# Kernel tuning notes

Hardware: AMD Instinct MI355X
Metric: run time of the kernel (lower is better)

## Reference

```python
import jax, jax.numpy as jnp
import numpy as np

B, I, H, MS, M = 8192, 1024, 1024, 64, 16
TAU = 1.0


def setup_inputs() -> dict:
    key = jax.random.key(0)
    ks = jax.random.split(key, 24)
    s = 0.02
    eps = 1e-6
    return {
        "x": jax.random.normal(ks[0], (B, I), jnp.float32),
        "h": jax.random.normal(ks[1], (B, H), jnp.float32),
        "c": jax.random.normal(ks[2], (B, H), jnp.float32),
        "memory": jax.random.normal(ks[3], (B, M, MS), jnp.float32),
        "u_gs": jax.random.uniform(ks[4], (B, M), jnp.float32, eps, 1.0 - eps),
        "u_a": jax.random.uniform(ks[5], (B, 1), jnp.float32, eps, 1.0 - eps),
        "u_b": jax.random.uniform(ks[6], (B, 1), jnp.float32, eps, 1.0 - eps),
        # pre-concatenated gate weights, matching torch.cat((W_x2*, W_h2*, W_c2*), 0)
        "W_i": jax.random.normal(ks[7], (I + 2 * H, H), jnp.float32) * s,
        "b_i": jnp.zeros((H,), jnp.float32),
        "W_f": jax.random.normal(ks[8], (I + 2 * H, H), jnp.float32) * s,
        "b_f": jnp.ones((H,), jnp.float32),
        "W_o": jax.random.normal(ks[9], (I + 2 * H, H), jnp.float32) * s,
        "b_o": jnp.zeros((H,), jnp.float32),
        "W_cand": jax.random.normal(ks[10], (I + H, H), jnp.float32) * s,
        "b_cand": jnp.zeros((H,), jnp.float32),
        "W_m": jax.random.normal(ks[11], (H, MS), jnp.float32) * s,
        "b_m": jnp.zeros((MS,), jnp.float32),
        "w_a_h": jax.random.normal(ks[12], (H, 1), jnp.float32) * s,
        "w_a_x": jax.random.normal(ks[13], (I, 1), jnp.float32) * s,
        "w_a_r": jax.random.normal(ks[14], (MS, 1), jnp.float32) * s,
        "w_b_h": jax.random.normal(ks[15], (H, 1), jnp.float32) * s,
        "w_b_x": jax.random.normal(ks[16], (I, 1), jnp.float32) * s,
        "w_b_r": jax.random.normal(ks[17], (MS, 1), jnp.float32) * s,
    }


def reference(x, h, c, memory, u_gs, u_a, u_b,
              W_i, b_i, W_f, b_f, W_o, b_o, W_cand, b_cand,
              W_m, b_m, w_a_h, w_a_x, w_a_r, w_b_h, w_b_x, w_b_r):
    # LSTM-style gates with peephole c in the concatenated input
    xhc = jnp.concatenate([x, h, c], axis=1)            # [B, I+2H]
    i = jax.nn.sigmoid(xhc @ W_i + b_i)
    f = jax.nn.sigmoid(xhc @ W_f + b_f)
    cp = jnp.tanh(jnp.concatenate([x, h], axis=1) @ W_cand + b_cand)
    c_new = f * c + i * cp
    o = jax.nn.sigmoid(jnp.concatenate([x, h, c_new], axis=1) @ W_o + b_o)
    h_new = o * jnp.tanh(c_new)

    # memory-slot attention with Gumbel-softmax sampling
    micro = h_new @ W_m + b_m                           # [B, MS]
    logits = jnp.einsum('bmk,bk->bm', memory, micro)    # [B, M]
    g = -jnp.log(-jnp.log(u_gs))                        # Gumbel(0,1)
    attn = jax.nn.softmax((logits + g) / TAU, axis=-1)  # sampled_locations
    sampled = jnp.einsum('bmk,bm->bk', memory, attn) + 1.0  # [B, MS]

    # gumbel-sigmoid (binary concrete) for alpha / beta
    la = jnp.log(u_a) - jnp.log1p(-u_a)
    lb = jnp.log(u_b) - jnp.log1p(-u_b)
    alpha = jax.nn.sigmoid((h_new @ w_a_h + x @ w_a_x + sampled @ w_a_r + la) / TAU)
    beta = jax.nn.sigmoid((h_new @ w_b_h + x @ w_b_x + sampled @ w_b_r + lb) / TAU)

    # [B, 2H+2]
    return jnp.concatenate([h_new, c_new, alpha, beta], axis=1)
```

## Files before the change

kernel.cpp:

```cpp
#include <hip/hip_runtime.h>

typedef __bf16 bfrag __attribute__((ext_vector_type(8)));
typedef float f32x4 __attribute__((ext_vector_type(4)));

#define GLDS16(g, l) __builtin_amdgcn_global_load_lds( \
    (__attribute__((address_space(1))) void*)(g),      \
    (__attribute__((address_space(3))) void*)(l), 16, 0, 0)

__device__ __forceinline__ float bf2f(ushort u) {
    return __uint_as_float(((unsigned)u) << 16);
}
__device__ __forceinline__ ushort f2bf(float f) {
    unsigned u = __float_as_uint(f);
    u += 0x7fff + ((u >> 16) & 1);
    return (ushort)(u >> 16);
}
__device__ __forceinline__ float sigmoidf_(float v) {
    return 1.0f / (1.0f + expf(-v));
}

struct TD { const float* src; ushort* dst; int src_ld; int dst_ld; int ktiles; int off; };
struct TA { TD d[6]; };

__global__ __launch_bounds__(256) void k_prep(const float* __restrict__ x,
                                              const float* __restrict__ h,
                                              const float* __restrict__ c,
                                              ushort* __restrict__ xhcb, TA a,
                                              const float* __restrict__ bi,
                                              const float* __restrict__ bf_,
                                              const float* __restrict__ bc,
                                              const float* __restrict__ bo,
                                              float* __restrict__ Biasf) {
    __shared__ float tile[64][65];
    int bid = blockIdx.x;
    int t = threadIdx.x;
    if (bid < 12288) {
        int idx = bid * 256 + t;
        int row = idx / 384;
        int c8 = (idx - row * 384) * 8;
        const float* s = (c8 < 1024) ? &x[(size_t)row * 1024 + c8]
                       : (c8 < 2048) ? &h[(size_t)row * 1024 + (c8 - 1024)]
                                     : &c[(size_t)row * 1024 + (c8 - 2048)];
        float4 va = *(const float4*)s;
        float4 vb = *(const float4*)(s + 4);
        ushort tmp[8] = {f2bf(va.x), f2bf(va.y), f2bf(va.z), f2bf(va.w),
                         f2bf(vb.x), f2bf(vb.y), f2bf(vb.z), f2bf(vb.w)};
        *(uint4*)&xhcb[(size_t)idx * 8] = *(uint4*)tmp;
    } else if (bid < 15120) {
        int tb = bid - 12288;
        int ri = 0;
#pragma unroll
        for (int i = 1; i < 6; ++i) ri = (tb >= a.d[i].off) ? i : ri;
        const float* src = a.d[ri].src;
        ushort* dst = a.d[ri].dst;
        int src_ld = a.d[ri].src_ld, dst_ld = a.d[ri].dst_ld;
        int local = tb - a.d[ri].off;
        int bx = local % a.d[ri].ktiles;
        int by = local / a.d[ri].ktiles;
        int k0 = bx * 64, n0 = by * 64;
        int c4 = (t & 15) * 4;
        int r = t >> 4;
#pragma unroll
        for (int i = 0; i < 4; ++i) {
            int rr = r + i * 16;
            float4 v = *(const float4*)&src[(size_t)(k0 + rr) * src_ld + n0 + c4];
            tile[rr][c4 + 0] = v.x; tile[rr][c4 + 1] = v.y;
            tile[rr][c4 + 2] = v.z; tile[rr][c4 + 3] = v.w;
        }
        __syncthreads();
        int kk8 = (t & 7) * 8;
        int nn = t >> 3;
#pragma unroll
        for (int i = 0; i < 2; ++i) {
            int n = nn + i * 32;
            ushort tmp[8];
#pragma unroll
            for (int j = 0; j < 8; ++j) tmp[j] = f2bf(tile[kk8 + j][n]);
            *(uint4*)&dst[(size_t)(n0 + n) * dst_ld + k0 + kk8] = *(uint4*)tmp;
        }
    } else {
        int idx = (bid - 15120) * 256 + t;
        int g = idx >> 10, n = idx & 1023;
        const float* s = (g == 0) ? bi : (g == 1) ? bf_ : (g == 2) ? bc : bo;
        Biasf[idx] = s[n];
    }
}

__global__ __launch_bounds__(512) void k_gemm1(const ushort* __restrict__ xhcb,
                                               const ushort* __restrict__ WT,
                                               const float* __restrict__ bias,
                                               ushort* __restrict__ Pre) {
    __shared__ __align__(16) ushort lds[2][32768];
    const int t = threadIdx.x;
    const int m0 = blockIdx.x * 256;
    const int by = blockIdx.y;
    const int n0 = by * 256;
    const int KTOT = (by < 8) ? 3072 : 2048;
    const int NT = KTOT >> 6;
    const int w = t >> 6, l = t & 63;
    const int wr = w >> 2, wc = w & 3;
    const int lane16 = l & 15, quad = l >> 4;
    const int r7 = lane16 & 7;
    const int rowt = t >> 3;
    const int kg = (t & 7) ^ (rowt & 7);
    const int brow_hi = rowt >> 5, brow_lo = rowt & 31;
    f32x4 acc[8][4] = {};

    const ushort* Ag = xhcb + (size_t)(m0 + rowt) * 3072 + kg * 8;
    const ushort* Bg = WT + (size_t)(n0 + brow_lo) * 3072 + kg * 8;

#define STAGE_A(BUF, PI, KT)                                                       \
    do {                                                                           \
        GLDS16(Ag + (size_t)((PI) * 64) * 3072 + (KT) * 64,                        \
               &lds[BUF][((PI) * 64) * 64] + t * 8);                               \
        GLDS16(Ag + (size_t)((PI) * 64 + 128) * 3072 + (KT) * 64,                  \
               &lds[BUF][((PI) * 64 + 128) * 64] + t * 8);                         \
    } while (0)

#define STAGE_B(BUF, PI, KT)                                                       \
    do {                                                                           \
        GLDS16(Bg + (size_t)((PI) * 32 + brow_hi * 64) * 3072 + (KT) * 64,         \
               &lds[BUF][16384 + ((PI) * 128) * 64] + t * 8);                      \
        GLDS16(Bg + (size_t)((PI) * 32 + (2 + brow_hi) * 64) * 3072 + (KT) * 64,   \
               &lds[BUF][16384 + ((PI) * 128 + 64) * 64] + t * 8);                 \
    } while (0)

#define LDAF(dst, QM, H)                                                                  \
    do {                                                                                  \
        _Pragma("unroll") for (int ii = 0; ii < 4; ++ii)                                  \
            dst[ii] = *(const bfrag*)&Acur[(wr * 128 + (QM) * 64 + ii * 16 + lane16) * 64 + \
                                           ((((H) * 4 + quad) ^ r7) * 8)];                \
    } while (0)

#define LDBF(dst, H)                                                                      \
    do {                                                                                  \
        _Pragma("unroll") for (int jj = 0; jj < 4; ++jj)                                  \
            dst[jj] = *(const bfrag*)&Bcur[((jj >> 1) * 128 + wc * 32 + (jj & 1) * 16 + lane16) * 64 + \
                                           ((((H) * 4 + quad) ^ r7) * 8)];                \
    } while (0)

#define MMH(QM, AH, BH)                                                                   \
    do {                                                                                  \
        __builtin_amdgcn_s_setprio(1);                                                    \
        _Pragma("unroll") for (int ii = 0; ii < 4; ++ii) {                                \
            _Pragma("unroll") for (int jj = 0; jj < 4; ++jj)                              \
                acc[(QM) * 4 + ii][jj] = __builtin_amdgcn_mfma_f32_16x16x32_bf16(         \
                    AH[ii], BH[jj], acc[(QM) * 4 + ii][jj], 0, 0, 0);                     \
        }                                                                                 \
        __builtin_amdgcn_s_setprio(0);                                                    \
    } while (0)

    STAGE_A(0, 0, 0); STAGE_B(0, 0, 0);
    STAGE_A(0, 1, 0); STAGE_B(0, 1, 0);
    STAGE_A(1, 0, 1); STAGE_B(1, 0, 1);
    asm volatile("s_waitcnt vmcnt(4)" ::: "memory");
    __builtin_amdgcn_s_barrier();

    for (int kt = 0; kt < NT; ++kt) {
        const int cur = kt & 1;
        const int nxt = cur ^ 1;
        const ushort* Acur = &lds[cur][0];
        const ushort* Bcur = Acur + 16384;
        bfrag a0h0[4], a0h1[4], a1h0[4], a1h1[4], bh0[4], bh1[4];
        LDAF(a0h0, 0, 0); LDBF(bh0, 0);
        LDAF(a0h1, 0, 1); LDBF(bh1, 1);
        if (kt + 1 < NT) STAGE_A(nxt, 1, kt + 1);
        MMH(0, a0h0, bh0);
        __builtin_amdgcn_s_barrier();
        LDAF(a1h0, 1, 0);
        if (kt + 1 < NT) STAGE_B(nxt, 1, kt + 1);
        MMH(0, a0h1, bh1);
        __builtin_amdgcn_s_barrier();
        LDAF(a1h1, 1, 1);
        if (kt + 2 < NT) STAGE_A(cur, 0, kt + 2);
        MMH(1, a1h0, bh0);
        __builtin_amdgcn_s_barrier();
        if (kt + 2 < NT) STAGE_B(cur, 0, kt + 2);
        MMH(1, a1h1, bh1);
        if (kt + 2 < NT) {
            asm volatile("s_waitcnt vmcnt(4)" ::: "memory");
        } else if (kt + 1 < NT) {
            asm volatile("s_waitcnt vmcnt(0)" ::: "memory");
        }
        __builtin_amdgcn_s_barrier();
    }
#undef MMH
#undef LDBF
#undef LDAF
#undef STAGE_B
#undef STAGE_A

#pragma unroll
    for (int i = 0; i < 8; ++i) {
#pragma unroll
        for (int jj = 0; jj < 4; ++jj) {
            int col = n0 + wc * 64 + (jj >> 1) * 32 + (jj & 1) * 16 + lane16;
            float bv = bias[col];
            int rbase = m0 + wr * 128 + i * 16 + quad * 4;
#pragma unroll
            for (int r = 0; r < 4; ++r)
                Pre[(size_t)(rbase + r) * 4096 + col] = f2bf(acc[i][jj][r] + bv);
        }
    }
}

__global__ __launch_bounds__(256) void k_cnew(const ushort* __restrict__ Pre,
                                              const float* __restrict__ cin,
                                              ushort* __restrict__ Cnewb,
                                              float* __restrict__ out) {
    int idx8 = blockIdx.x * 256 + threadIdx.x;
    int b = idx8 >> 7;
    int n8 = (idx8 & 127) * 8;
    uint4 vi = *(const uint4*)(Pre + (size_t)b * 4096 + n8);
    uint4 vf = *(const uint4*)(Pre + (size_t)b * 4096 + 1024 + n8);
    uint4 vc = *(const uint4*)(Pre + (size_t)b * 4096 + 2048 + n8);
    float4 c0 = *(const float4*)(cin + (size_t)b * 1024 + n8);
    float4 c1 = *(const float4*)(cin + (size_t)b * 1024 + n8 + 4);
    const ushort* pi = (const ushort*)&vi;
    const ushort* pf = (const ushort*)&vf;
    const ushort* pc = (const ushort*)&vc;
    float cv[8] = {c0.x, c0.y, c0.z, c0.w, c1.x, c1.y, c1.z, c1.w};
    float cn[8];
    ushort cb[8];
#pragma unroll
    for (int j = 0; j < 8; ++j) {
        float iv = sigmoidf_(bf2f(pi[j]));
        float fv = sigmoidf_(bf2f(pf[j]));
        float cp = tanhf(bf2f(pc[j]));
        cn[j] = fv * cv[j] + iv * cp;
        cb[j] = f2bf(cn[j]);
    }
    *(uint4*)(Cnewb + (size_t)b * 1024 + n8) = *(uint4*)cb;
    float* orow = out + (size_t)b * 2050 + 1024 + n8;
#pragma unroll
    for (int j = 0; j < 4; ++j)
        *(float2*)(orow + j * 2) = make_float2(cn[j * 2], cn[j * 2 + 1]);
}

__global__ __launch_bounds__(256) void k_gemm2(const ushort* __restrict__ Cnewb,
                                               const ushort* __restrict__ WoCT,
                                               const ushort* __restrict__ Pre,
                                               ushort* __restrict__ Hnewb,
                                               float* __restrict__ out) {
    __shared__ __align__(16) ushort As[128 * 64];
    __shared__ __align__(16) ushort Bs[128 * 64];
    int t = threadIdx.x;
    int m0 = blockIdx.x * 128, n0 = blockIdx.y * 128;
    int w = t >> 6, l = t & 63;
    int wm = (w & 1) * 64, wn = (w >> 1) * 64;
    int lane16 = l & 15, quad = l >> 4;
    int rowt = t >> 3;
    int kg = (t & 7) ^ (rowt & 7);
    int r7 = lane16 & 7;
    f32x4 acc[4][4] = {};

    const ushort* Abase = Cnewb + (size_t)(m0 + rowt) * 1024 + kg * 8;
    const ushort* Bbase = WoCT + (size_t)(n0 + rowt) * 1024 + kg * 8;

    for (int k0 = 0; k0 < 1024; k0 += 64) {
#pragma unroll
        for (int q = 0; q < 4; ++q)
            GLDS16(Abase + (size_t)q * 32 * 1024 + k0, As + q * 2048 + t * 8);
#pragma unroll
        for (int q = 0; q < 4; ++q)
            GLDS16(Bbase + (size_t)q * 32 * 1024 + k0, Bs + q * 2048 + t * 8);
        __syncthreads();
#pragma unroll
        for (int hh = 0; hh < 2; ++hh) {
            int slot8 = ((hh * 4 + quad) ^ r7) * 8;
            bfrag af[4], bfr[4];
#pragma unroll
            for (int i = 0; i < 4; ++i) {
                af[i]  = *(const bfrag*)&As[(wm + i * 16 + lane16) * 64 + slot8];
                bfr[i] = *(const bfrag*)&Bs[(wn + i * 16 + lane16) * 64 + slot8];
            }
#pragma unroll
            for (int i = 0; i < 4; ++i)
#pragma unroll
                for (int j = 0; j < 4; ++j)
                    acc[i][j] = __builtin_amdgcn_mfma_f32_16x16x32_bf16(af[i], bfr[j], acc[i][j], 0, 0, 0);
        }
        __syncthreads();
    }
#pragma unroll
    for (int i = 0; i < 4; ++i) {
#pragma unroll
        for (int j = 0; j < 4; ++j) {
            int col = n0 + wn + j * 16 + lane16;
            int rbase = m0 + wm + i * 16 + quad * 4;
#pragma unroll
            for (int r = 0; r < 4; ++r) {
                int row = rbase + r;
                float opre = acc[i][j][r] + bf2f(Pre[(size_t)row * 4096 + 3072 + col]);
                float o = sigmoidf_(opre);
                float cnv = bf2f(Cnewb[(size_t)row * 1024 + col]);
                float hv = o * tanhf(cnv);
                Hnewb[(size_t)row * 1024 + col] = f2bf(hv);
                out[(size_t)row * 2050 + col] = hv;
            }
        }
    }
}

__global__ __launch_bounds__(256) void k_attn(
    const ushort* __restrict__ Hnewb, const float* __restrict__ outr,
    const float* __restrict__ x, const float* __restrict__ memory,
    const float* __restrict__ u_gs, const float* __restrict__ u_a,
    const float* __restrict__ u_b, const ushort* __restrict__ WmT,
    const float* __restrict__ b_m,
    const float* __restrict__ w_a_h, const float* __restrict__ w_a_x,
    const float* __restrict__ w_a_r, const float* __restrict__ w_b_h,
    const float* __restrict__ w_b_x, const float* __restrict__ w_b_r,
    float* __restrict__ out) {
    __shared__ float sMicro[16 * 64];
    __shared__ float sAttn[16 * 16];
    __shared__ float sSamp[16 * 64];

    int b0 = blockIdx.x * 16;
    int t = threadIdx.x;
    int w = t >> 6, l = t & 63;
    int lane16 = l & 15, quad = l >> 4;

    {
        f32x4 acc = {0.f, 0.f, 0.f, 0.f};
        const ushort* Ab = Hnewb + (size_t)(b0 + lane16) * 1024 + quad * 8;
        const ushort* Bb = WmT + (size_t)(w * 16 + lane16) * 1024 + quad * 8;
#pragma unroll 4
        for (int k0 = 0; k0 < 1024; k0 += 32) {
            bfrag av = *(const bfrag*)(Ab + k0);
            bfrag bv = *(const bfrag*)(Bb + k0);
            acc = __builtin_amdgcn_mfma_f32_16x16x32_bf16(av, bv, acc, 0, 0, 0);
        }
        float bm = b_m[w * 16 + lane16];
#pragma unroll
        for (int r = 0; r < 4; ++r)
            sMicro[(quad * 4 + r) * 64 + w * 16 + lane16] = acc[r] + bm;
    }
    __syncthreads();

    {
        int r = t >> 4, m = t & 15;
        const float4* mem4 = (const float4*)(memory + (size_t)(b0 + r) * 1024 + m * 64);
        float lg = 0.f;
#pragma unroll
        for (int k4 = 0; k4 < 16; ++k4) {
            float4 mv = mem4[k4];
            const float* sm = &sMicro[r * 64 + k4 * 4];
            lg += mv.x * sm[0] + mv.y * sm[1] + mv.z * sm[2] + mv.w * sm[3];
        }
        float u = u_gs[(b0 + r) * 16 + m];
        float z = lg - logf(-logf(u));
        float zm = z;
        for (int off = 8; off; off >>= 1) zm = fmaxf(zm, __shfl_xor(zm, off, 16));
        float p = expf(z - zm);
        float ps = p;
        for (int off = 8; off; off >>= 1) ps += __shfl_xor(ps, off, 16);
        sAttn[r * 16 + m] = p / ps;
    }
    __syncthreads();

#pragma unroll
    for (int q = 0; q < 4; ++q) {
        int r = w * 4 + q;
        const float* mem = memory + (size_t)(b0 + r) * 1024 + l;
        float s = 0.f;
#pragma unroll
        for (int m = 0; m < 16; ++m) s += sAttn[r * 16 + m] * mem[m * 64];
        sSamp[r * 64 + l] = s + 1.0f;
    }
    __syncthreads();

    {
        int r = t >> 4, s16 = t & 15;
        size_t hoff = (size_t)(b0 + r) * 2050;
        size_t xoff = (size_t)(b0 + r) * 1024;
        float za = 0.f, zb = 0.f;
        for (int kk = 0; kk < 64; ++kk) {
            int k = s16 + kk * 16;
            float hv = outr[hoff + k];
            float xv = x[xoff + k];
            za += hv * w_a_h[k] + xv * w_a_x[k];
            zb += hv * w_b_h[k] + xv * w_b_x[k];
        }
#pragma unroll
        for (int k = s16 * 4; k < s16 * 4 + 4; ++k) {
            float sv = sSamp[r * 64 + k];
            za += sv * w_a_r[k];
            zb += sv * w_b_r[k];
        }
        for (int off = 8; off; off >>= 1) {
            za += __shfl_xor(za, off, 16);
            zb += __shfl_xor(zb, off, 16);
        }
        if (s16 == 0) {
            float ua = u_a[b0 + r];
            float ub = u_b[b0 + r];
            float la = logf(ua) - log1pf(-ua);
            float lb = logf(ub) - log1pf(-ub);
            out[(size_t)(b0 + r) * 2050 + 2048] = sigmoidf_(za + la);
            out[(size_t)(b0 + r) * 2050 + 2049] = sigmoidf_(zb + lb);
        }
    }
}

extern "C" void kernel_launch(void* const* d_in, const int* in_sizes, int n_in,
                              void* d_out, int out_size, void* d_ws, size_t ws_size,
                              hipStream_t stream) {
    const float* x      = (const float*)d_in[0];
    const float* h      = (const float*)d_in[1];
    const float* c      = (const float*)d_in[2];
    const float* memory = (const float*)d_in[3];
    const float* u_gs   = (const float*)d_in[4];
    const float* u_a    = (const float*)d_in[5];
    const float* u_b    = (const float*)d_in[6];
    const float* W_i    = (const float*)d_in[7];
    const float* b_i    = (const float*)d_in[8];
    const float* W_f    = (const float*)d_in[9];
    const float* b_f    = (const float*)d_in[10];
    const float* W_o    = (const float*)d_in[11];
    const float* b_o    = (const float*)d_in[12];
    const float* W_cand = (const float*)d_in[13];
    const float* b_cand = (const float*)d_in[14];
    const float* W_m    = (const float*)d_in[15];
    const float* b_m    = (const float*)d_in[16];
    const float* w_a_h  = (const float*)d_in[17];
    const float* w_a_x  = (const float*)d_in[18];
    const float* w_a_r  = (const float*)d_in[19];
    const float* w_b_h  = (const float*)d_in[20];
    const float* w_b_x  = (const float*)d_in[21];
    const float* w_b_r  = (const float*)d_in[22];
    float* out = (float*)d_out;

    char* ws = (char*)d_ws;
    ushort* WT    = (ushort*)(ws);
    ushort* WoCT  = (ushort*)(ws + 25165824);
    ushort* Pre   = (ushort*)(ws + 27262976);
    ushort* xhcb  = (ushort*)(ws + 94371840);
    float*  Biasf = (float*)(ws + 144703488);
    ushort* WmT   = (ushort*)(ws + 144719872);
    ushort* Cnewb = xhcb;
    ushort* Hnewb = WT;

    TA ta;
    ta.d[0] = {W_i,                       WT,                        1024, 3072, 48, 0};
    ta.d[1] = {W_f,                       WT + (size_t)1024 * 3072,  1024, 3072, 48, 768};
    ta.d[2] = {W_cand,                    WT + (size_t)2048 * 3072,  1024, 3072, 32, 1536};
    ta.d[3] = {W_o,                       WT + (size_t)3072 * 3072,  1024, 3072, 32, 2048};
    ta.d[4] = {W_o + (size_t)2048 * 1024, WoCT,                      1024, 1024, 16, 2560};
    ta.d[5] = {W_m,                       WmT,                         64, 1024, 16, 2816};

    k_prep<<<15136, 256, 0, stream>>>(x, h, c, xhcb, ta, b_i, b_f, b_cand, b_o, Biasf);

    k_gemm1<<<dim3(32, 16), 512, 0, stream>>>(xhcb, WT, Biasf, Pre);
    k_cnew<<<4096, 256, 0, stream>>>(Pre, c, Cnewb, out);
    k_gemm2<<<dim3(64, 8), 256, 0, stream>>>(Cnewb, WoCT, Pre, Hnewb, out);
    k_attn<<<512, 256, 0, stream>>>(Hnewb, out, x, memory, u_gs, u_a, u_b, WmT, b_m,
                                    w_a_h, w_a_x, w_a_r, w_b_h, w_b_x, w_b_r, out);
}
```

Measured before the change: 476.2 us.

## Prefetch next k-tile's first A/B fragments during last MFMA phase

Moves the LDS reads of the first A and B fragment set for the next k-tile into the final phase of the current iteration, so they overlap with the last MFMA block instead of stalling at loop start. The vmcnt wait is moved earlier and loosened to guarantee the next buffer's data has landed before those reads. This adds live registers for fragments carried across iterations and depends on the revised wait counts being correct for the staging order.

```diff
diff --git a/kernel.cpp b/kernel.cpp
--- a/kernel.cpp
+++ b/kernel.cpp
@@ -105,6 +105,8 @@
     const int kg = (t & 7) ^ (rowt & 7);
     const int brow_hi = rowt >> 5, brow_lo = rowt & 31;
     f32x4 acc[8][4] = {};
+    bfrag a0h0[4], bh0[4];
+    bfrag a0h1[4], bh1[4], a1h0[4], a1h1[4];
 
     const ushort* Ag = xhcb + (size_t)(m0 + rowt) * 3072 + kg * 8;
     const ushort* Bg = WT + (size_t)(n0 + brow_lo) * 3072 + kg * 8;
@@ -125,18 +127,18 @@
                &lds[BUF][16384 + ((PI) * 128 + 64) * 64] + t * 8);                 \
     } while (0)
 
-#define LDAF(dst, QM, H)                                                                  \
+#define LDAF(dst, BASE, QM, H)                                                            \
     do {                                                                                  \
         _Pragma("unroll") for (int ii = 0; ii < 4; ++ii)                                  \
-            dst[ii] = *(const bfrag*)&Acur[(wr * 128 + (QM) * 64 + ii * 16 + lane16) * 64 + \
-                                           ((((H) * 4 + quad) ^ r7) * 8)];                \
+            dst[ii] = *(const bfrag*)&(BASE)[(wr * 128 + (QM) * 64 + ii * 16 + lane16) * 64 + \
+                                             ((((H) * 4 + quad) ^ r7) * 8)];              \
     } while (0)
 
-#define LDBF(dst, H)                                                                      \
+#define LDBF(dst, BASE, H)                                                                \
     do {                                                                                  \
         _Pragma("unroll") for (int jj = 0; jj < 4; ++jj)                                  \
-            dst[jj] = *(const bfrag*)&Bcur[((jj >> 1) * 128 + wc * 32 + (jj & 1) * 16 + lane16) * 64 + \
-                                           ((((H) * 4 + quad) ^ r7) * 8)];                \
+            dst[jj] = *(const bfrag*)&(BASE)[((jj >> 1) * 128 + wc * 32 + (jj & 1) * 16 + lane16) * 64 + \
+                                             ((((H) * 4 + quad) ^ r7) * 8)];              \
     } while (0)
 
 #define MMH(QM, AH, BH)                                                                   \
@@ -155,33 +157,43 @@
     STAGE_A(1, 0, 1); STAGE_B(1, 0, 1);
     asm volatile("s_waitcnt vmcnt(4)" ::: "memory");
     __builtin_amdgcn_s_barrier();
+    {
+        const ushort* A0b = &lds[0][0];
+        const ushort* B0b = A0b + 16384;
+        LDAF(a0h0, A0b, 0, 0);
+        LDBF(bh0, B0b, 0);
+    }
 
     for (int kt = 0; kt < NT; ++kt) {
         const int cur = kt & 1;
         const int nxt = cur ^ 1;
         const ushort* Acur = &lds[cur][0];
         const ushort* Bcur = Acur + 16384;
-        bfrag a0h0[4], a0h1[4], a1h0[4], a1h1[4], bh0[4], bh1[4];
-        LDAF(a0h0, 0, 0); LDBF(bh0, 0);
-        LDAF(a0h1, 0, 1); LDBF(bh1, 1);
+        const ushort* An = &lds[nxt][0];
+        const ushort* Bn = An + 16384;
+        LDAF(a0h1, Acur, 0, 1); LDBF(bh1, Bcur, 1);
         if (kt + 1 < NT) STAGE_A(nxt, 1, kt + 1);
         MMH(0, a0h0, bh0);
         __builtin_amdgcn_s_barrier();
-        LDAF(a1h0, 1, 0);
+        LDAF(a1h0, Acur, 1, 0);
         if (kt + 1 < NT) STAGE_B(nxt, 1, kt + 1);
         MMH(0, a0h1, bh1);
         __builtin_amdgcn_s_barrier();
-        LDAF(a1h1, 1, 1);
+        LDAF(a1h1, Acur, 1, 1);
         if (kt + 2 < NT) STAGE_A(cur, 0, kt + 2);
         MMH(1, a1h0, bh0);
+        if (kt + 2 < NT) {
+            asm volatile("s_waitcnt vmcnt(6)" ::: "memory");
+        } else if (kt + 1 < NT) {
+            asm volatile("s_waitcnt vmcnt(4)" ::: "memory");
+        }
         __builtin_amdgcn_s_barrier();
         if (kt + 2 < NT) STAGE_B(cur, 0, kt + 2);
+        if (kt + 1 < NT) {
+            LDAF(a0h0, An, 0, 0);
+            LDBF(bh0, Bn, 0);
+        }
         MMH(1, a1h1, bh1);
-        if (kt + 2 < NT) {
-            asm volatile("s_waitcnt vmcnt(4)" ::: "memory");
-        } else if (kt + 1 < NT) {
-            asm volatile("s_waitcnt vmcnt(0)" ::: "memory");
-        }
         __builtin_amdgcn_s_barrier();
     }
 #undef MMH
```

Measured after the change: 489.3 us. 1.03x slower.
